# Performance work log

Hardware: AMD Instinct MI355X
Metric: run time of the kernel (lower is better)

## Reference

```python
import jax, jax.numpy as jnp
import numpy as np
from jax import lax

EPS = 1e-5

def conv2d(x, w, groups=1, pad=0):
    return lax.conv_general_dilated(
        x, w, window_strides=(1, 1), padding=[(pad, pad), (pad, pad)],
        dimension_numbers=('NCHW', 'OIHW', 'NCHW'), feature_group_count=groups)

def setup_inputs() -> dict:
    key = jax.random.key(0)
    ks = jax.random.split(key, 10)
    B, C, H, W = 8, 64, 128, 128
    s = 0.05
    f32 = jnp.float32
    return {
        'x': jax.random.normal(ks[0], (B, C, H, W), f32),
        # key_embed: Conv2d(64,64,3,groups=8,bias=False) -> weight [64, 64/8, 3, 3]
        'w_key': jax.random.normal(ks[1], (64, 8, 3, 3), f32) * s,
        # embed[0]: Conv2d(128,32,1,groups=2,bias=False) -> [32, 128/2, 1, 1]
        'w_e1': jax.random.normal(ks[2], (32, 64, 1, 1), f32) * s,
        # embed[2]: Conv2d(32,72,1,groups=2,bias=True) -> [72, 32/2, 1, 1]
        'w_e2': jax.random.normal(ks[3], (72, 16, 1, 1), f32) * s,
        'b_e2': jax.random.normal(ks[4], (72,), f32) * s,
        # GroupNorm(num_groups=8, num_channels=72) affine params
        'gn_w': jnp.ones((72,), f32),
        'gn_b': jnp.zeros((72,), f32),
        # conv1x1: Conv2d(64,64,1,groups=2,bias=False) -> [64, 32, 1, 1]
        'w_c1': jax.random.normal(ks[5], (64, 32, 1, 1), f32) * s,
        # conv_du: Conv2d(64,4,1,bias=False), Conv2d(4,64,1,bias=False)
        'w_du1': jax.random.normal(ks[6], (4, 64, 1, 1), f32) * s,
        'w_du2': jax.random.normal(ks[7], (64, 4, 1, 1), f32) * s,
    }

def reference(x, w_key, w_e1, w_e2, b_e2, gn_w, gn_b, w_c1, w_du1, w_du2):
    B, C, H, W = x.shape  # C == 64
    KK = 9                # kernel_size^2
    # key embedding: grouped 3x3 conv + ReLU
    k = jax.nn.relu(conv2d(x, w_key, groups=8, pad=1))
    # interleave x and k along channels: view of [B,64,2,H,W] -> [B,128,H,W]
    qk = jnp.stack([x, k], axis=2).reshape(B, 2 * C, H, W)
    # dynamic kernel generation (embed)
    w = jax.nn.relu(conv2d(qk, w_e1, groups=2))
    w = conv2d(w, w_e2, groups=2) + b_e2[None, :, None, None]  # [B,72,H,W]
    # GroupNorm(8, 72): normalize over (channels-in-group, H, W)
    wg = w.reshape(B, 8, 9, H, W)
    m = wg.mean(axis=(2, 3, 4), keepdims=True)
    v = wg.var(axis=(2, 3, 4), keepdims=True)
    w = ((wg - m) * lax.rsqrt(v + EPS)).reshape(B, 72, H, W)
    w = w * gn_w[None, :, None, None] + gn_b[None, :, None, None]
    # per-pixel kernels: [B*2, 4, 9, H, W]
    w = w.reshape(B * 2, 4, KK, H, W)
    # value path
    xv = conv2d(x, w_c1, groups=2).reshape(B * 2, 32, H, W)
    # unfold 3x3 patches with zero padding 1 -> [B*2, 32, 9, H, W]
    xp = jnp.pad(xv, ((0, 0), (0, 0), (1, 1), (1, 1)))
    patches = jnp.stack(
        [xp[:, :, i:i + H, j:j + W] for i in range(3) for j in range(3)], axis=2)
    # share_planes=8: 8 channels share each kernel -> [B*2, 4, 8, 9, H, W]
    patches = patches.reshape(B * 2, 4, 8, KK, H, W)
    out = jnp.einsum('bgckhw,bgkhw->bgchw', patches, w)  # local conv
    out = out.reshape(B, C, H, W)
    # channel attention
    y = out.mean(axis=(2, 3))                 # [B, 64]
    y = jax.nn.relu(y @ w_du1[:, :, 0, 0].T)  # [B, 4]
    y = jax.nn.sigmoid(y @ w_du2[:, :, 0, 0].T)  # [B, 64]
    return out * y[:, :, None, None]
```

## Files before the change

### kernel.cpp

```cpp
#include <hip/hip_runtime.h>
#include <math.h>

#define Hd 128
#define Wd 128
#define HW 16384

__device__ __forceinline__ float wred(float v) {
  #pragma unroll
  for (int o = 32; o > 0; o >>= 1) v += __shfl_down(v, o, 64);
  return v;
}

__global__ __launch_bounds__(256) void k_fused(const float* __restrict__ x,
                                               const float* __restrict__ wkey,
                                               const float* __restrict__ we1,
                                               const float* __restrict__ we2,
                                               const float* __restrict__ be2,
                                               const float* __restrict__ wc1,
                                               float* __restrict__ xv,
                                               float* __restrict__ wpre,
                                               float* __restrict__ spart) {
  __shared__ float xt[8][18][24];
  __shared__ float sred2[4][8];
  const int tid = threadIdx.x;
  const int tx = tid & 15, ty = tid >> 4;
  const int b = blockIdx.y, s = blockIdx.z;
  const int h0 = (blockIdx.x >> 3) * 16, w0 = (blockIdx.x & 7) * 16;
  const int p = ((h0 + ty) << 7) + (w0 + tx);
  float xc[32], kc[32];
  for (int g = 0; g < 4; ++g) {
    for (int i = tid; i < 8 * 324; i += 256) {
      int ch = i / 324, r = i - ch * 324;
      int yy = r / 18, xx = r - yy * 18;
      int gh = h0 + yy - 1, gw = w0 + xx - 1;
      float v = 0.f;
      if (gh >= 0 && gh < Hd && gw >= 0 && gw < Wd)
        v = x[((long)(b * 64 + 32 * s + 8 * g + ch) << 14) + (gh << 7) + gw];
      xt[ch][yy][xx] = v;
    }
    __syncthreads();
    float kacc[8] = {0.f, 0.f, 0.f, 0.f, 0.f, 0.f, 0.f, 0.f};
    const float* wg = wkey + (4 * s + g) * 576;
    #pragma unroll
    for (int ich = 0; ich < 8; ++ich) {
      float nb[9];
      #pragma unroll
      for (int rr = 0; rr < 3; ++rr)
        #pragma unroll
        for (int cc = 0; cc < 3; ++cc)
          nb[rr * 3 + cc] = xt[ich][ty + rr][tx + cc];
      xc[8 * g + ich] = nb[4];
      #pragma unroll
      for (int oc = 0; oc < 8; ++oc) {
        const float* wr = wg + oc * 72 + ich * 9;
        #pragma unroll
        for (int k9 = 0; k9 < 9; ++k9) kacc[oc] += wr[k9] * nb[k9];
      }
    }
    #pragma unroll
    for (int oc = 0; oc < 8; ++oc) kc[8 * g + oc] = fmaxf(kacc[oc], 0.f);
    __syncthreads();
  }
  float* xvp = xv + ((long)(b * HW + p)) * 64 + 32 * s;
  #pragma unroll
  for (int o4 = 0; o4 < 8; ++o4) {
    float va[4];
    #pragma unroll
    for (int oo = 0; oo < 4; ++oo) {
      const float* wr = wc1 + (32 * s + 4 * o4 + oo) * 32;
      float a = 0.f;
      #pragma unroll
      for (int j = 0; j < 32; ++j) a += wr[j] * xc[j];
      va[oo] = a;
    }
    ((float4*)xvp)[o4] = make_float4(va[0], va[1], va[2], va[3]);
  }
  float w1a[16];
  #pragma unroll
  for (int o = 0; o < 16; ++o) {
    const float* wr = we1 + (16 * s + o) * 64;
    float a = 0.f;
    #pragma unroll
    for (int j = 0; j < 32; ++j) a += wr[2 * j] * xc[j] + wr[2 * j + 1] * kc[j];
    w1a[o] = fmaxf(a, 0.f);
  }
  float* wpp = wpre + ((long)(b * HW + p)) * 72 + 36 * s;
  #pragma unroll
  for (int gl = 0; gl < 4; ++gl) {
    float lgs = 0.f, lgq = 0.f;
    #pragma unroll
    for (int kk = 0; kk < 9; ++kk) {
      const int oc2 = 36 * s + gl * 9 + kk;
      const float* wr = we2 + oc2 * 16;
      float a = be2[oc2];
      #pragma unroll
      for (int ic = 0; ic < 16; ++ic) a += wr[ic] * w1a[ic];
      wpp[gl * 9 + kk] = a;
      lgs += a;
      lgq += a * a;
    }
    float r1 = wred(lgs), r2 = wred(lgq);
    if ((tid & 63) == 0) {
      sred2[tid >> 6][2 * gl] = r1;
      sred2[tid >> 6][2 * gl + 1] = r2;
    }
  }
  __syncthreads();
  if (tid < 8) {
    float a = sred2[0][tid] + sred2[1][tid] + sred2[2][tid] + sred2[3][tid];
    spart[blockIdx.x * 128 + b * 16 + s * 8 + tid] = a;
  }
}

__global__ __launch_bounds__(256) void k_local(const float* __restrict__ xv,
                                               const float* __restrict__ wpre,
                                               const float* __restrict__ spart,
                                               const float* __restrict__ gnw,
                                               const float* __restrict__ gnb,
                                               float* __restrict__ out,
                                               float* __restrict__ part) {
  __shared__ float xt[8][34][24];
  __shared__ float sminv[2];
  const int tid = threadIdx.x;
  const int tx = tid & 15, ty = tid >> 4;
  const int z = blockIdx.z;
  const int b2 = z >> 2, g = z & 3;
  const int t = b2 & 1, b = b2 >> 1;
  const int gg = 4 * t + g;
  const int h0 = blockIdx.y * 32, w0 = blockIdx.x * 16;
  for (int i = tid; i < 612; i += 256) {
    int yy = i / 18, xx = i - yy * 18;
    int gh = h0 + yy - 1, gw = w0 + xx - 1;
    float4 v0 = make_float4(0.f, 0.f, 0.f, 0.f), v1 = v0;
    if (gh >= 0 && gh < Hd && gw >= 0 && gw < Wd) {
      const float4* src = (const float4*)(xv + ((long)(b * HW) + (gh << 7) + gw) * 64 +
                                          32 * t + 8 * g);
      v0 = src[0];
      v1 = src[1];
    }
    xt[0][yy][xx] = v0.x; xt[1][yy][xx] = v0.y; xt[2][yy][xx] = v0.z; xt[3][yy][xx] = v0.w;
    xt[4][yy][xx] = v1.x; xt[5][yy][xx] = v1.y; xt[6][yy][xx] = v1.z; xt[7][yy][xx] = v1.w;
  }
  if (tid < 64) {
    const float* sp = spart + tid * 128 + (b * 8 + gg) * 2;
    float sv = sp[0], qv = sp[1];
    #pragma unroll
    for (int o = 32; o > 0; o >>= 1) {
      sv += __shfl_down(sv, o, 64);
      qv += __shfl_down(qv, o, 64);
    }
    if (tid == 0) {
      const float N = 9.f * (float)HW;
      float mm = sv / N;
      float var = qv / N - mm * mm;
      sminv[0] = mm;
      sminv[1] = rsqrtf(var + 1e-5f);
    }
  }
  __syncthreads();
  const float m = sminv[0];
  const float inv = sminv[1];
  const int p0 = ((h0 + 2 * ty) << 7) + (w0 + tx);
  const int p1 = p0 + 128;
  const float* w0p = wpre + ((long)(b * HW + p0)) * 72 + 36 * t + 9 * g;
  const float* w1p = wpre + ((long)(b * HW + p1)) * 72 + 36 * t + 9 * g;
  float wn0[9], wn1[9];
  #pragma unroll
  for (int kk = 0; kk < 9; ++kk) {
    const int ch72 = 36 * t + 9 * g + kk;
    const float sc = inv * gnw[ch72], sh = gnb[ch72] - m * inv * gnw[ch72];
    wn0[kk] = w0p[kk] * sc + sh;
    wn1[kk] = w1p[kk] * sc + sh;
  }
  const int prow = (blockIdx.y * 8 + blockIdx.x) * 4 + (tid >> 6);
  #pragma unroll
  for (int cc = 0; cc < 8; ++cc) {
    float nb[12];
    #pragma unroll
    for (int rr = 0; rr < 4; ++rr)
      #pragma unroll
      for (int ccol = 0; ccol < 3; ++ccol)
        nb[rr * 3 + ccol] = xt[cc][2 * ty + rr][tx + ccol];
    float o0 = 0.f, o1 = 0.f;
    #pragma unroll
    for (int dy = 0; dy < 3; ++dy)
      #pragma unroll
      for (int dx = 0; dx < 3; ++dx) {
        o0 += wn0[dy * 3 + dx] * nb[dy * 3 + dx];
        o1 += wn1[dy * 3 + dx] * nb[(dy + 1) * 3 + dx];
      }
    const int ch512 = b2 * 32 + g * 8 + cc;
    out[((long)ch512 << 14) + p0] = o0;
    out[((long)ch512 << 14) + p1] = o1;
    float os = wred(o0 + o1);
    if ((tid & 63) == 0) part[prow * 512 + ch512] = os;
  }
}

__global__ void k_ca(const float* __restrict__ part, const float* __restrict__ du1,
                     const float* __restrict__ du2, float* __restrict__ ys) {
  __shared__ float sy[8][64];
  __shared__ float sy4[8][4];
  const int tid = threadIdx.x;
  const int b = tid >> 6, c = tid & 63;
  float acc = 0.f;
  #pragma unroll 8
  for (int r = 0; r < 128; ++r) acc += part[r * 512 + tid];
  sy[b][c] = acc * (1.f / (float)HW);
  __syncthreads();
  if (tid < 32) {
    int bb = tid >> 2, j = tid & 3;
    float a = 0.f;
    for (int c2 = 0; c2 < 64; ++c2) a += sy[bb][c2] * du1[j * 64 + c2];
    sy4[bb][j] = fmaxf(a, 0.f);
  }
  __syncthreads();
  float z = 0.f;
  #pragma unroll
  for (int j = 0; j < 4; ++j) z += sy4[b][j] * du2[c * 4 + j];
  ys[tid] = 1.f / (1.f + expf(-z));
}

__global__ __launch_bounds__(256) void k_scale(float* __restrict__ out,
                                               const float* __restrict__ ys) {
  const long i4 = (long)blockIdx.x * 256 + threadIdx.x;
  const long e = i4 * 4;
  const int bc = (int)(e >> 14);
  const float s = ys[bc];
  float4* o = (float4*)out;
  float4 v = o[i4];
  v.x *= s; v.y *= s; v.z *= s; v.w *= s;
  o[i4] = v;
}

extern "C" void kernel_launch(void* const* d_in, const int* in_sizes, int n_in,
                              void* d_out, int out_size, void* d_ws, size_t ws_size,
                              hipStream_t stream) {
  const float* x    = (const float*)d_in[0];
  const float* wkey = (const float*)d_in[1];
  const float* we1  = (const float*)d_in[2];
  const float* we2  = (const float*)d_in[3];
  const float* be2  = (const float*)d_in[4];
  const float* gnw  = (const float*)d_in[5];
  const float* gnb  = (const float*)d_in[6];
  const float* wc1  = (const float*)d_in[7];
  const float* du1  = (const float*)d_in[8];
  const float* du2  = (const float*)d_in[9];
  float* out = (float*)d_out;
  float* ws = (float*)d_ws;

  float* xv   = ws;
  float* wpre = ws + 8388608;
  float* part = ws + 17825792;
  float* spart = part + 65536;
  float* ys   = spart + 8192;

  k_fused<<<dim3(64, 8, 2), 256, 0, stream>>>(x, wkey, we1, we2, be2, wc1, xv, wpre, spart);
  k_local<<<dim3(8, 4, 64), 256, 0, stream>>>(xv, wpre, spart, gnw, gnb, out, part);
  k_ca<<<1, 512, 0, stream>>>(part, du1, du2, ys);
  k_scale<<<8192, 256, 0, stream>>>(out, ys);
}
```

Baseline: 230.8 us.

## Switch xv and wpre intermediates from pixel-major to channel-planar layout

The intermediate value tensor xv and the pre-norm kernel tensor wpre move from pixel-major (HWC-like) storage to channel-planar NCHW storage in both producer and consumer kernels. Each thread's per-channel store and load now lands on consecutive pixels across a wavefront, so accesses coalesce instead of being strided by 64 or 72 floats. In exchange, the float4 vector loads in the local-conv tile fill become scalar loads with more index arithmetic. The g loop is also marked for full unrolling.

After: 227.9 us. About the same (-1.3%).

```diff
diff --git a/kernel.cpp b/kernel.cpp
--- a/kernel.cpp
+++ b/kernel.cpp
@@ -28,6 +28,7 @@
   const int h0 = (blockIdx.x >> 3) * 16, w0 = (blockIdx.x & 7) * 16;
   const int p = ((h0 + ty) << 7) + (w0 + tx);
   float xc[32], kc[32];
+  #pragma unroll
   for (int g = 0; g < 4; ++g) {
     for (int i = tid; i < 8 * 324; i += 256) {
       int ch = i / 324, r = i - ch * 324;
@@ -61,19 +62,13 @@
     for (int oc = 0; oc < 8; ++oc) kc[8 * g + oc] = fmaxf(kacc[oc], 0.f);
     __syncthreads();
   }
-  float* xvp = xv + ((long)(b * HW + p)) * 64 + 32 * s;
-  #pragma unroll
-  for (int o4 = 0; o4 < 8; ++o4) {
-    float va[4];
-    #pragma unroll
-    for (int oo = 0; oo < 4; ++oo) {
-      const float* wr = wc1 + (32 * s + 4 * o4 + oo) * 32;
-      float a = 0.f;
-      #pragma unroll
-      for (int j = 0; j < 32; ++j) a += wr[j] * xc[j];
-      va[oo] = a;
-    }
-    ((float4*)xvp)[o4] = make_float4(va[0], va[1], va[2], va[3]);
+  #pragma unroll 4
+  for (int o = 0; o < 32; ++o) {
+    const float* wr = wc1 + (32 * s + o) * 32;
+    float a = 0.f;
+    #pragma unroll
+    for (int j = 0; j < 32; ++j) a += wr[j] * xc[j];
+    xv[((long)(b * 64 + 32 * s + o) << 14) + p] = a;
   }
   float w1a[16];
   #pragma unroll
@@ -84,7 +79,6 @@
     for (int j = 0; j < 32; ++j) a += wr[2 * j] * xc[j] + wr[2 * j + 1] * kc[j];
     w1a[o] = fmaxf(a, 0.f);
   }
-  float* wpp = wpre + ((long)(b * HW + p)) * 72 + 36 * s;
   #pragma unroll
   for (int gl = 0; gl < 4; ++gl) {
     float lgs = 0.f, lgq = 0.f;
@@ -95,7 +89,7 @@
       float a = be2[oc2];
       #pragma unroll
       for (int ic = 0; ic < 16; ++ic) a += wr[ic] * w1a[ic];
-      wpp[gl * 9 + kk] = a;
+      wpre[((long)(b * 72 + oc2) << 14) + p] = a;
       lgs += a;
       lgq += a * a;
     }
@@ -128,18 +122,14 @@
   const int t = b2 & 1, b = b2 >> 1;
   const int gg = 4 * t + g;
   const int h0 = blockIdx.y * 32, w0 = blockIdx.x * 16;
-  for (int i = tid; i < 612; i += 256) {
-    int yy = i / 18, xx = i - yy * 18;
+  for (int i = tid; i < 8 * 612; i += 256) {
+    int ch = i / 612, r = i - ch * 612;
+    int yy = r / 18, xx = r - yy * 18;
     int gh = h0 + yy - 1, gw = w0 + xx - 1;
-    float4 v0 = make_float4(0.f, 0.f, 0.f, 0.f), v1 = v0;
-    if (gh >= 0 && gh < Hd && gw >= 0 && gw < Wd) {
-      const float4* src = (const float4*)(xv + ((long)(b * HW) + (gh << 7) + gw) * 64 +
-                                          32 * t + 8 * g);
-      v0 = src[0];
-      v1 = src[1];
-    }
-    xt[0][yy][xx] = v0.x; xt[1][yy][xx] = v0.y; xt[2][yy][xx] = v0.z; xt[3][yy][xx] = v0.w;
-    xt[4][yy][xx] = v1.x; xt[5][yy][xx] = v1.y; xt[6][yy][xx] = v1.z; xt[7][yy][xx] = v1.w;
+    float v = 0.f;
+    if (gh >= 0 && gh < Hd && gw >= 0 && gw < Wd)
+      v = xv[((long)(b * 64 + t * 32 + g * 8 + ch) << 14) + (gh << 7) + gw];
+    xt[ch][yy][xx] = v;
   }
   if (tid < 64) {
     const float* sp = spart + tid * 128 + (b * 8 + gg) * 2;
@@ -162,15 +152,14 @@
   const float inv = sminv[1];
   const int p0 = ((h0 + 2 * ty) << 7) + (w0 + tx);
   const int p1 = p0 + 128;
-  const float* w0p = wpre + ((long)(b * HW + p0)) * 72 + 36 * t + 9 * g;
-  const float* w1p = wpre + ((long)(b * HW + p1)) * 72 + 36 * t + 9 * g;
   float wn0[9], wn1[9];
   #pragma unroll
   for (int kk = 0; kk < 9; ++kk) {
     const int ch72 = 36 * t + 9 * g + kk;
+    const long base = ((long)(b * 72 + ch72) << 14);
     const float sc = inv * gnw[ch72], sh = gnb[ch72] - m * inv * gnw[ch72];
-    wn0[kk] = w0p[kk] * sc + sh;
-    wn1[kk] = w1p[kk] * sc + sh;
+    wn0[kk] = wpre[base + p0] * sc + sh;
+    wn1[kk] = wpre[base + p1] * sc + sh;
   }
   const int prow = (blockIdx.y * 8 + blockIdx.x) * 4 + (tid >> 6);
   #pragma unroll
```
